# Kernel optimization log

Hardware: AMD Instinct MI355X
Metric: run time of the kernel (lower is better)

The kernel has to match this reference:

```python
import jax, jax.numpy as jnp
import numpy as np

B, HH, WW, C = 8, 56, 56, 192
DEPTH = 2
D_IN = 384      # ssm_ratio=2.0 * d_model
R = 12          # dt_rank = ceil(192/16)
HID = 768
L = HH * WW
EPS = 1e-5

PNAMES = ("norm1_w", "norm1_b", "in_proj_w", "conv_w", "conv_b", "x_proj_w",
          "dt_proj_w", "dt_proj_b", "A_log", "Ds", "out_norm_w", "out_norm_b",
          "out_proj_w", "norm2_w", "norm2_b", "fc1_w", "fc1_b", "fc2_w", "fc2_b")


def _mst_bfs_np(fm):
    """Per-image MST (Kruskal) on the 4-connected grid with cosine-distance
    edge weights mapped through exp (MinimumSpanningTree('Cosine', torch.exp)),
    then BFS from node 0. Returns (bfs order, parent-of-ordered-node)."""
    fm = np.asarray(fm, np.float32)
    Bn, H, W, Cc = fm.shape
    Ln = H * W
    idx_out = np.zeros((Bn, Ln), np.int32)
    par_out = np.zeros((Bn, Ln), np.int32)
    ids = np.arange(Ln).reshape(H, W)
    e_u = np.concatenate([ids[:, :-1].ravel(), ids[:-1, :].ravel()])
    e_v = np.concatenate([ids[:, 1:].ravel(), ids[1:, :].ravel()])
    for b in range(Bn):
        f = fm[b].reshape(Ln, Cc)
        nrm = np.linalg.norm(f, axis=1) + 1e-8
        cos = (f[e_u] * f[e_v]).sum(1) / (nrm[e_u] * nrm[e_v])
        wgt = np.exp(1.0 - cos)
        order = np.argsort(wgt, kind="stable")
        uf = np.arange(Ln)
        def find(a):
            while uf[a] != a:
                uf[a] = uf[uf[a]]
                a = uf[a]
            return a
        adj = [[] for _ in range(Ln)]
        cnt = 0
        for e in order:
            u, v = int(e_u[e]), int(e_v[e])
            ru, rv = find(u), find(v)
            if ru != rv:
                uf[ru] = rv
                adj[u].append(v)
                adj[v].append(u)
                cnt += 1
                if cnt == Ln - 1:
                    break
        bfs = np.zeros(Ln, np.int32)
        par = np.zeros(Ln, np.int32)
        visited = np.zeros(Ln, bool)
        visited[0] = True
        head, tail = 0, 1
        while head < tail:
            u = int(bfs[head])
            for v in adj[u]:
                if not visited[v]:
                    visited[v] = True
                    bfs[tail] = v
                    par[tail] = u
                    tail += 1
            head += 1
        idx_out[b] = bfs
        par_out[b] = par
    return idx_out, par_out


def _mst_bfs(x):
    shp = jax.ShapeDtypeStruct((x.shape[0], x.shape[1] * x.shape[2]), jnp.int32)
    return jax.pure_callback(_mst_bfs_np, (shp, shp), jax.lax.stop_gradient(x))


def _ln(x, w, b):
    mu = jnp.mean(x, -1, keepdims=True)
    var = jnp.mean((x - mu) ** 2, -1, keepdims=True)
    return (x - mu) * jax.lax.rsqrt(var + EPS) * w + b


def _tree_scan(feat, w, bfs_idx, bfs_par):
    # feat, w: (B, L, D); bfs_idx/bfs_par: (B, L) int32.
    # Pass 1 (leaf->root): S[p] += w[n] * S[n] in reverse BFS order.
    # Pass 2 (root->leaf): H[n] = S[n] + w[n] * (H[p] - w[n] * S[n]).
    Bn = feat.shape[0]
    bi = jnp.arange(Bn)

    def p1(S, np_):
        n, p = np_
        S = S.at[bi, p].add(w[bi, n] * S[bi, n])
        return S, None

    xs1 = (bfs_idx[:, 1:][:, ::-1].T, bfs_par[:, 1:][:, ::-1].T)
    S, _ = jax.lax.scan(p1, feat, xs1)

    def p2(Hc, np_):
        n, p = np_
        wn, sn = w[bi, n], S[bi, n]
        Hc = Hc.at[bi, n].set(sn + wn * (Hc[bi, p] - wn * sn))
        return Hc, None

    xs2 = (bfs_idx[:, 1:].T, bfs_par[:, 1:].T)
    Hh, _ = jax.lax.scan(p2, S, xs2)
    return Hh


def _layer(x, p, tree):
    bfs_idx, bfs_par = tree
    Bn = x.shape[0]
    # --- Tree_SSM branch (pre-norm) ---
    xn = _ln(x, p["norm1_w"], p["norm1_b"])
    xz = xn @ p["in_proj_w"].T                     # (B,H,W,2*D_IN)
    xs, z = jnp.split(xz, 2, axis=-1)
    xs = jax.lax.conv_general_dilated(
        xs, p["conv_w"], (1, 1), "SAME",
        dimension_numbers=("NHWC", "HWIO", "NHWC"),
        feature_group_count=D_IN) + p["conv_b"]    # depthwise 3x3
    u = jax.nn.silu(xs).reshape(Bn, L, D_IN)       # (B,L,D)
    x_dbl = u @ p["x_proj_w"].T                    # (B,L,R+2), d_state=1
    dts = jax.nn.softplus(x_dbl[..., :R] @ p["dt_proj_w"].T + p["dt_proj_b"])
    Bs, Cs = x_dbl[..., R:R + 1], x_dbl[..., R + 1:R + 2]
    A = -jnp.exp(p["A_log"][:, 0])                 # (D,)
    w = jnp.exp(dts * A)                           # edge decay to parent
    feat = dts * Bs * u                            # delta * B * u
    Hh = _tree_scan(feat, w, bfs_idx, bfs_par)
    y = (Cs * Hh + p["Ds"] * u).reshape(Bn, HH, WW, D_IN)
    y = _ln(y, p["out_norm_w"], p["out_norm_b"]) * jax.nn.silu(z)
    x = x + y @ p["out_proj_w"].T
    # --- MLP branch ---
    h = _ln(x, p["norm2_w"], p["norm2_b"])
    h = jax.nn.gelu(h @ p["fc1_w"].T + p["fc1_b"], approximate=False)
    return x + h @ p["fc2_w"].T + p["fc2_b"]


def setup_inputs() -> dict:
    key = jax.random.key(0)
    ks = jax.random.split(key, 12)
    n = jax.random.normal
    return {
        "x": n(ks[0], (B, HH, WW, C), jnp.float32),
        "norm1_w": jnp.ones((DEPTH, C)), "norm1_b": jnp.zeros((DEPTH, C)),
        "in_proj_w": n(ks[1], (DEPTH, 2 * D_IN, C)) * 0.02,
        "conv_w": n(ks[2], (DEPTH, 3, 3, 1, D_IN)) * 0.05,
        "conv_b": jnp.zeros((DEPTH, D_IN)),
        "x_proj_w": n(ks[3], (DEPTH, R + 2, D_IN)) * 0.02,
        "dt_proj_w": n(ks[4], (DEPTH, D_IN, R)) * 0.05,
        "dt_proj_b": n(ks[5], (DEPTH, D_IN)) * 0.1,
        "A_log": jnp.log(0.5 + jax.random.uniform(ks[6], (DEPTH, D_IN, 1))),
        "Ds": jax.random.uniform(ks[7], (DEPTH, D_IN)),
        "out_norm_w": jnp.ones((DEPTH, D_IN)), "out_norm_b": jnp.zeros((DEPTH, D_IN)),
        "out_proj_w": n(ks[8], (DEPTH, C, D_IN)) * 0.02,
        "norm2_w": jnp.ones((DEPTH, C)), "norm2_b": jnp.zeros((DEPTH, C)),
        "fc1_w": n(ks[9], (DEPTH, HID, C)) * 0.02, "fc1_b": jnp.zeros((DEPTH, HID)),
        "fc2_w": n(ks[10], (DEPTH, C, HID)) * 0.02, "fc2_b": jnp.zeros((DEPTH, C)),
        "fnorm_w": jnp.ones((C,)), "fnorm_b": jnp.zeros((C,)),
    }


def reference(x, norm1_w, norm1_b, in_proj_w, conv_w, conv_b, x_proj_w,
              dt_proj_w, dt_proj_b, A_log, Ds, out_norm_w, out_norm_b,
              out_proj_w, norm2_w, norm2_b, fc1_w, fc1_b, fc2_w, fc2_b,
              fnorm_w, fnorm_b):
    pvals = (norm1_w, norm1_b, in_proj_w, conv_w, conv_b, x_proj_w, dt_proj_w,
             dt_proj_b, A_log, Ds, out_norm_w, out_norm_b, out_proj_w, norm2_w,
             norm2_b, fc1_w, fc1_b, fc2_w, fc2_b)
    for i in range(DEPTH):
        pl = {k: v[i] for k, v in zip(PNAMES, pvals)}
        tree = _mst_bfs(x)  # input-adaptive MST, recomputed per layer
        x = _layer(x, pl, tree)
    return _ln(x, fnorm_w, fnorm_b)
```

## Files before the change

kernel.cpp:

```cpp
#include <hip/hip_runtime.h>
#include <math.h>

#define NB 8
#define NC 192
#define DIN 384
#define NL 3136
#define ROWS (NB*NL)
#define NE 6160
#define NHID 768

typedef unsigned short u16;
typedef unsigned int u32;
typedef unsigned long long u64;
typedef __attribute__((ext_vector_type(8))) short bh8;
typedef __attribute__((ext_vector_type(4))) float f4;

typedef __attribute__((address_space(1))) const void gl_as1;
typedef __attribute__((address_space(3))) void gl_as3;
#define GL16(g, l) __builtin_amdgcn_global_load_lds((gl_as1*)(const void*)(g), (gl_as3*)(void*)(l), 16, 0, 0)

__device__ __forceinline__ float wredsum(float v){
  v += __shfl_xor(v, 1, 64); v += __shfl_xor(v, 2, 64); v += __shfl_xor(v, 4, 64);
  v += __shfl_xor(v, 8, 64); v += __shfl_xor(v, 16, 64); v += __shfl_xor(v, 32, 64);
  return v;
}
__device__ __forceinline__ void edge_decode(int e, int& u, int& v){
  if (e < 3080){ int h = e/55, w = e - h*55; u = h*56 + w; v = u + 1; }
  else { int e2 = e - 3080; int h = e2/56, w = e2 - h*56; u = h*56 + w; v = u + 56; }
}
__device__ __forceinline__ float siluf(float x){ return x / (1.0f + expf(-x)); }
__device__ __forceinline__ float sofplus(float x){ return fmaxf(x, 0.0f) + log1pf(expf(-fabsf(x))); }
__device__ __forceinline__ float geluf(float x){ return 0.5f * x * (1.0f + erff(x * 0.70710678118654752f)); }
__device__ __forceinline__ u16 f2bf(float x){
  u32 u = __float_as_uint(x);
  u32 r = (u + 0x7fffu + ((u >> 16) & 1u)) >> 16;
  return (u16)r;
}
__device__ __forceinline__ float bf2f(u16 h){ return __uint_as_float(((u32)h) << 16); }

__global__ __launch_bounds__(256) void keysln_kernel(const float* __restrict__ x,
    const float* __restrict__ g, const float* __restrict__ bt,
    u16* __restrict__ lnout, u64* __restrict__ keys,
    const float* __restrict__ ipw, const float* __restrict__ opw,
    const float* __restrict__ f1w, const float* __restrict__ f2w,
    u16* __restrict__ ipo, u16* __restrict__ opo, u16* __restrict__ f1o, u16* __restrict__ f2o){
  int bid = blockIdx.x;
  int lane = threadIdx.x & 63;
  if (bid < 6272){
    int gw = (int)((bid * 256u + threadIdx.x) >> 6);
    const float* r = x + (size_t)gw * NC;
    float v[3]; float s = 0.f;
#pragma unroll
    for (int j = 0; j < 3; ++j){ v[j] = r[lane + 64*j]; s += v[j]; }
    s = wredsum(s);
    float mu = s * (1.0f / NC);
    float q = 0.f;
#pragma unroll
    for (int j = 0; j < 3; ++j){ float dd = v[j] - mu; q += dd*dd; }
    q = wredsum(q);
    float rs = rsqrtf(q * (1.0f / NC) + 1e-5f);
    u16* o = lnout + (size_t)gw * NC;
#pragma unroll
    for (int j = 0; j < 3; ++j){
      int dch = lane + 64*j;
      o[dch] = f2bf((v[j] - mu) * rs * g[dch] + bt[dch]);
    }
  } else if (bid < 18592){
    int gw = (int)(((bid - 6272) * 256u + threadIdx.x) >> 6);
    if (gw >= NB * NE) return;
    int b = gw / NE, e = gw - b * NE;
    int u, v; edge_decode(e, u, v);
    const float* ru = x + ((size_t)b * NL + u) * NC;
    const float* rv = x + ((size_t)b * NL + v) * NC;
    float s = 0.f, su = 0.f, sv = 0.f;
#pragma unroll
    for (int j = 0; j < 3; ++j){
      float a = ru[lane + 64*j], c = rv[lane + 64*j];
      s += a * c; su += a * a; sv += c * c;
    }
    s = wredsum(s);
    su = wredsum(su);
    sv = wredsum(sv);
    if (lane == 0){
      float nu = sqrtf(su) + 1e-8f;
      float nv = sqrtf(sv) + 1e-8f;
      float cosv = s / (nu * nv);
      float wgt = expf(1.0f - cosv);
      keys[(size_t)b*NE + e] = ((u64)__float_as_uint(wgt) << 32) | (u64)(u32)e;
    }
  } else {
    int wb = bid - 18592;
    const float* W; u16* o; int K; int nk; int base;
    if (wb < 576){ W = ipw; o = ipo; K = 192; nk = 768*192; base = wb; }
    else if (wb < 864){ W = opw; o = opo; K = 384; nk = 192*384; base = wb - 576; }
    else if (wb < 1440){ W = f1w; o = f1o; K = 192; nk = 768*192; base = wb - 864; }
    else { W = f2w; o = f2o; K = 768; nk = 192*768; base = wb - 1440; }
    int i = base*256 + threadIdx.x;
    if (i >= nk) return;
    int r = i / K, c = i - r*K;
    float v = W[i];
    u16 hi = f2bf(v);
    o[(size_t)r * 2 * K + c] = hi;
    o[(size_t)r * 2 * K + K + c] = f2bf(v - bf2f(hi));
  }
}

__device__ void tree_body(char* sm, int b, const u64* __restrict__ keys_g,
      int* __restrict__ order_g, int* __restrict__ parpos_g, int* __restrict__ pos_g,
      int* __restrict__ lvl_g, int* __restrict__ nlev_g){
  const int t = threadIdx.x;
  const int NT = 256;
  u64* best   = (u64*)sm;
  u16* parent = (u16*)(sm + 25088);
  u16* comp   = (u16*)(sm + 31360);
  u16* mstU   = (u16*)(sm + 37632);
  u16* mstV   = (u16*)(sm + 43904);
  u32* cnts   = (u32*)(sm + 56448);
  u16* adjl4  = (u16*)sm;
  u32* deg    = (u32*)(sm + 25088);

  const u64* kb = keys_g + (size_t)b * NE;
  for (int v = t; v < NL; v += NT) parent[v] = (u16)v;
  if (t == 0){ cnts[0] = 0; cnts[3] = 0xffffffffu; }
  __syncthreads();

  u32 gpass = 0;
  for (int round = 0; round < 24; ++round){
    for (int it = 0; it < 12; ++it){
      bool ch = false;
      for (int c0 = 0; c0 < NL; c0 += NT*4){
        int vv[4]; u16 pv[4]; int nb2 = 0;
#pragma unroll
        for (int j = 0; j < 4; ++j){ int v = c0 + t + j*NT; if (v < NL){ vv[nb2] = v; pv[nb2] = parent[v]; ++nb2; } }
        u16 gp[4];
        for (int j = 0; j < nb2; ++j) gp[j] = parent[pv[j]];
        for (int j = 0; j < nb2; ++j){ if (gp[j] != pv[j]){ parent[vv[j]] = gp[j]; ch = true; } }
      }
      bool docheck = (it & 1);
      if (docheck && ch) cnts[3] = gpass;
      __syncthreads();
      if (docheck){
        u32 seen = cnts[3];
        __syncthreads();
        u32 cur = gpass; ++gpass;
        if (seen != cur) break;
      }
    }
    for (int v = t; v < NL; v += NT){ comp[v] = parent[v]; best[v] = ~0ull; }
    if (t == 0) cnts[2] = 0;
    __syncthreads();
    for (int c0 = 0; c0 < NE; c0 += NT*8){
      int ee[8]; int eu[8], ev[8]; u16 cu[8], cv[8]; u64 kk[8]; int nb2 = 0;
#pragma unroll
      for (int j = 0; j < 8; ++j){
        int e = c0 + t + j*NT;
        if (e < NE){ ee[nb2] = e; int u, v; edge_decode(e, u, v); eu[nb2] = u; ev[nb2] = v; ++nb2; }
      }
      for (int j = 0; j < nb2; ++j){ cu[j] = comp[eu[j]]; cv[j] = comp[ev[j]]; }
      for (int j = 0; j < nb2; ++j){ kk[j] = kb[ee[j]]; }
      for (int j = 0; j < nb2; ++j){
        if (cu[j] != cv[j]){
          atomicMin(&best[cu[j]], kk[j]);
          atomicMin(&best[cv[j]], kk[j]);
        }
      }
    }
    __syncthreads();
    for (int c0 = 0; c0 < NL; c0 += NT*4){
      int rr[4]; u64 bk[4]; int nb2 = 0;
#pragma unroll
      for (int j = 0; j < 4; ++j){ int r = c0 + t + j*NT; if (r < NL){ rr[nb2] = r; ++nb2; } }
      u16 cr[4];
      for (int j = 0; j < nb2; ++j) cr[j] = comp[rr[j]];
      for (int j = 0; j < nb2; ++j) bk[j] = (cr[j] == (u16)rr[j]) ? best[rr[j]] : ~0ull;
      int uu[4], vv2[4]; u16 ru2[4], rv2[4];
      for (int j = 0; j < nb2; ++j){
        if (bk[j] != ~0ull){ int e = (int)(u32)bk[j]; edge_decode(e, uu[j], vv2[j]); }
      }
      for (int j = 0; j < nb2; ++j){
        if (bk[j] != ~0ull){ ru2[j] = comp[uu[j]]; rv2[j] = comp[vv2[j]]; }
      }
      for (int j = 0; j < nb2; ++j){
        if (bk[j] != ~0ull){
          int r = rr[j];
          u16 other = (ru2[j] == (u16)r) ? rv2[j] : ru2[j];
          bool mutual = (best[other] == bk[j]);
          if (!mutual || (u16)r < other){
            parent[r] = other;
            u32 id = atomicAdd(&cnts[0], 1);
            mstU[id] = (u16)uu[j]; mstV[id] = (u16)vv2[j];
            cnts[2] = 1;
          }
        }
      }
    }
    __syncthreads();
    if (cnts[0] >= (u32)(NL - 1) || cnts[2] == 0) break;
  }
  __syncthreads();

  const int nm = NL - 1;
  for (int v = t; v < NL; v += NT){
    deg[v] = 0;
    *(u64*)&adjl4[v*4] = 0xffffffffffffffffull;
  }
  __syncthreads();
  for (int c0 = 0; c0 < nm; c0 += NT*4){
    int uu[4], vv2[4]; int nb2 = 0;
#pragma unroll
    for (int j = 0; j < 4; ++j){
      int i = c0 + t + j*NT;
      if (i < nm){ uu[nb2] = mstU[i]; vv2[nb2] = mstV[i]; ++nb2; }
    }
    for (int j = 0; j < nb2; ++j){
      u32 s1 = atomicAdd(&deg[uu[j]], 1); adjl4[uu[j]*4 + s1] = (u16)vv2[j];
      u32 s2 = atomicAdd(&deg[vv2[j]], 1); adjl4[vv2[j]*4 + s2] = (u16)uu[j];
    }
  }
  __syncthreads();

  const int NARC = 2 * (NL - 1);
  u16*  arcB  = (u16*)(sm + 37632);
  u16*  nxt   = (u16*)(sm + 43908);
  u16*  rankA = (u16*)(sm + 25088);
  short* S16  = (short*)(sm + 43908);
  u16*  parA  = (u16*)(sm + 43908);
  u32*  hist  = (u32*)(sm + 25088);
  u16*  posA  = (u16*)(sm + 37632);
  u16*  dep   = (u16*)(sm + 56448);
  u32*  wsum  = (u32*)(sm + 62720);
  const int lane = t & 63, wv = t >> 6;

  {
    int dloc[13]; int st = 0;
#pragma unroll
    for (int j = 0; j < 13; ++j){
      int v = t*13 + j;
      dloc[j] = (v < NL) ? (int)deg[v] : 0;
      st += dloc[j];
    }
    int inc = st;
#pragma unroll
    for (int off = 1; off < 64; off <<= 1){
      int sh = __shfl_up(inc, off, 64);
      if (lane >= off) inc += sh;
    }
    if (lane == 63) wsum[wv] = (u32)inc;
    __syncthreads();
    int woff = 0;
    for (int k = 0; k < 4; ++k) if (k < wv) woff += (int)wsum[k];
    int run = woff + inc - st;
#pragma unroll
    for (int j = 0; j < 13; ++j){
      int v = t*13 + j;
      if (v < NL) arcB[v] = (u16)run;
      run += dloc[j];
    }
    if (t == 255) arcB[NL] = (u16)run;
  }
  __syncthreads();

  for (int idx = t; idx < NL*4; idx += NT){
    int u = idx >> 2, sl = idx & 3;
    int v = (int)adjl4[idx];
    if (v != 0xffff){
      int dv = (int)(arcB[v+1] - arcB[v]);
      int rs = 0;
#pragma unroll
      for (int j = 0; j < 4; ++j) if ((int)adjl4[v*4+j] == u) rs = j;
      int ns = rs + 1; if (ns >= dv) ns = 0;
      nxt[arcB[u] + sl] = (u16)(arcB[v] + ns);
    }
  }
  __syncthreads();
  for (int a = t; a < NARC; a += NT){
    if (nxt[a] == 0) nxt[a] = 0xffff;
  }
  __syncthreads();

  for (int a = t; a < NARC; a += NT) rankA[a] = (nxt[a] == 0xffff) ? (u16)0 : (u16)1;
  __syncthreads();
  for (int it = 0; it < 13; ++it){
    u16 nn[25], rr2[25];
#pragma unroll
    for (int k = 0; k < 25; ++k){
      int a = t + k*NT;
      nn[k] = 0xfffe; rr2[k] = 0;
      if (a < NARC){
        u16 n = nxt[a];
        if (n != 0xffff){ rr2[k] = rankA[n]; nn[k] = nxt[n]; }
      }
    }
    __syncthreads();
#pragma unroll
    for (int k = 0; k < 25; ++k){
      int a = t + k*NT;
      if (a < NARC && nn[k] != 0xfffe){
        rankA[a] = (u16)(rankA[a] + rr2[k]);
        nxt[a] = nn[k];
      }
    }
    __syncthreads();
  }

  for (int idx = t; idx < NL*4; idx += NT){
    int u = idx >> 2, sl = idx & 3;
    int v = (int)adjl4[idx];
    if (v != 0xffff){
      int a  = arcB[u] + sl;
      int rs = 0;
#pragma unroll
      for (int j = 0; j < 4; ++j) if ((int)adjl4[v*4+j] == u) rs = j;
      int ar = arcB[v] + rs;
      bool down = rankA[a] > rankA[ar];
      int pt = (NARC - 1) - (int)rankA[a];
      S16[pt] = down ? (short)1 : (short)-1;
    }
  }
  __syncthreads();

  {
    int base = t * 25;
    int vals[25]; int st = 0;
#pragma unroll
    for (int j = 0; j < 25; ++j){
      int i = base + j;
      vals[j] = (i < NARC) ? (int)S16[i] : 0;
      st += vals[j];
    }
    int inc = st;
#pragma unroll
    for (int off = 1; off < 64; off <<= 1){
      int sh = __shfl_up(inc, off, 64);
      if (lane >= off) inc += sh;
    }
    if (lane == 63) wsum[wv] = (u32)inc;
    __syncthreads();
    int woff = 0;
    for (int k = 0; k < 4; ++k) if (k < wv) woff += (int)wsum[k];
    int run = woff + inc - st;
#pragma unroll
    for (int j = 0; j < 25; ++j){
      int i = base + j;
      run += vals[j];
      if (i < NARC) S16[i] = (short)run;
    }
  }
  __syncthreads();

  if (t == 0) dep[0] = 0;
  for (int idx = t; idx < NL*4; idx += NT){
    int u = idx >> 2, sl = idx & 3;
    int v = (int)adjl4[idx];
    if (v != 0xffff){
      int a  = arcB[u] + sl;
      int rs = 0;
#pragma unroll
      for (int j = 0; j < 4; ++j) if ((int)adjl4[v*4+j] == u) rs = j;
      int ar = arcB[v] + rs;
      if (rankA[a] > rankA[ar]){
        int pt = (NARC - 1) - (int)rankA[a];
        dep[v] = (u16)S16[pt];
      }
    }
  }
  __syncthreads();

  if (t == 0) parA[0] = 0;
  for (int idx = t; idx < NL*4; idx += NT){
    int u = idx >> 2, sl = idx & 3;
    int v = (int)adjl4[idx];
    if (v != 0xffff){
      int a  = arcB[u] + sl;
      int rs = 0;
#pragma unroll
      for (int j = 0; j < 4; ++j) if ((int)adjl4[v*4+j] == u) rs = j;
      int ar = arcB[v] + rs;
      if (rankA[a] > rankA[ar]) parA[v] = (u16)u;
    }
  }
  __syncthreads();

  for (int i = t; i < NL; i += NT) hist[i] = 0;
  __syncthreads();
  int mloc = 0;
  for (int v = t; v < NL; v += NT){
    int dv = (int)dep[v];
    atomicAdd(&hist[dv], 1u);
    if (dv > mloc) mloc = dv;
  }
#pragma unroll
  for (int off = 1; off < 64; off <<= 1){
    int o = __shfl_xor(mloc, off, 64);
    if (o > mloc) mloc = o;
  }
  __syncthreads();
  if (lane == 0) wsum[wv] = (u32)mloc;
  __syncthreads();
  int maxd = 0;
  for (int k = 0; k < 4; ++k){ int x = (int)wsum[k]; if (x > maxd) maxd = x; }
  int nlev = maxd + 1;
  __syncthreads();

  {
    int hloc[13]; int st = 0;
#pragma unroll
    for (int j = 0; j < 13; ++j){
      int i2 = t*13 + j;
      hloc[j] = (i2 < NL) ? (int)hist[i2] : 0;
      st += hloc[j];
    }
    int inc = st;
#pragma unroll
    for (int off = 1; off < 64; off <<= 1){
      int sh = __shfl_up(inc, off, 64);
      if (lane >= off) inc += sh;
    }
    if (lane == 63) wsum[wv] = (u32)inc;
    __syncthreads();
    int woff = 0;
    for (int k = 0; k < 4; ++k) if (k < wv) woff += (int)wsum[k];
    int run = woff + inc - st;
#pragma unroll
    for (int j = 0; j < 13; ++j){
      int i2 = t*13 + j;
      int h = hloc[j];
      if (i2 < NL) hist[i2] = (u32)run;
      run += h;
    }
  }
  __syncthreads();
  for (int i = t; i < nlev; i += NT) lvl_g[b*3200 + i] = (int)hist[i];
  if (t == 0){ lvl_g[b*3200 + nlev] = NL; nlev_g[b] = nlev; }
  __syncthreads();

  for (int v = t; v < NL; v += NT){
    u32 p = atomicAdd(&hist[(int)dep[v]], 1u);
    posA[v] = (u16)p;
  }
  __syncthreads();

  for (int v = t; v < NL; v += NT){
    int p = (int)posA[v];
    order_g[b*NL + p] = v;
    pos_g[b*NL + v] = p;
    parpos_g[b*NL + p] = (int)posA[parA[v]];
  }
}

__device__ void inproj_body(char* sm, int bid, const u16* __restrict__ Ap, const u16* __restrict__ Wp,
                            float* __restrict__ Cm, float* __restrict__ C2){
  const int K = 192, K2 = 384;
  short* Ah = (short*)sm;
  short* Wh = (short*)(sm + 16384);
  short* Wl = (short*)(sm + 32768);
  const int bn = (bid % 6) * 128, bm = (bid / 6) * 128;
  const int tid = threadIdx.x, lane = tid & 63, wid = tid >> 6;
  const int wr = wid >> 1, wc = wid & 1;
  f4 acc[4][4];
#pragma unroll
  for (int mf = 0; mf < 4; ++mf)
#pragma unroll
    for (int nf = 0; nf < 4; ++nf) acc[mf][nf] = (f4){0.f,0.f,0.f,0.f};

  for (int k0 = 0; k0 < K; k0 += 64){
#pragma unroll
    for (int j = 0; j < 4; ++j){
      int isb = wid*4 + j;
      int r = isb*8 + (lane >> 3);
      int c = lane & 7;
      const u16* src = Ap + (size_t)(bm + r) * K + k0 + ((c ^ (r & 7)) << 3);
      GL16(src, &Ah[isb*512]);
    }
#pragma unroll
    for (int j = 0; j < 4; ++j){
      int isb = wid*4 + j;
      int r = isb*8 + (lane >> 3);
      int c = lane & 7;
      const u16* src = Wp + (size_t)(bn + r) * K2 + k0 + ((c ^ (r & 7)) << 3);
      GL16(src,     &Wh[isb*512]);
      GL16(src + K, &Wl[isb*512]);
    }
    __syncthreads();
#pragma unroll
    for (int kk = 0; kk < 2; ++kk){
      bh8 whf[4], wlf[4], ahf[4];
#pragma unroll
      for (int nf = 0; nf < 4; ++nf){
        int rw = wc*64 + nf*16 + (lane & 15);
        int c = kk*4 + (lane >> 4);
        int ad = rw*64 + ((c ^ (rw & 7)) * 8);
        whf[nf] = *(const bh8*)&Wh[ad];
        wlf[nf] = *(const bh8*)&Wl[ad];
      }
#pragma unroll
      for (int mf = 0; mf < 4; ++mf){
        int ra = wr*64 + mf*16 + (lane & 15);
        int c = kk*4 + (lane >> 4);
        int ad = ra*64 + ((c ^ (ra & 7)) * 8);
        ahf[mf] = *(const bh8*)&Ah[ad];
      }
#pragma unroll
      for (int mf = 0; mf < 4; ++mf)
#pragma unroll
        for (int nf = 0; nf < 4; ++nf){
          acc[mf][nf] = __builtin_amdgcn_mfma_f32_16x16x32_bf16(ahf[mf], whf[nf], acc[mf][nf], 0, 0, 0);
          acc[mf][nf] = __builtin_amdgcn_mfma_f32_16x16x32_bf16(ahf[mf], wlf[nf], acc[mf][nf], 0, 0, 0);
        }
    }
    __syncthreads();
  }
  const int cb = bn + wc*64;
#pragma unroll
  for (int mf = 0; mf < 4; ++mf){
    int row = bm + wr*64 + mf*16 + (lane >> 4)*4;
#pragma unroll
    for (int nf = 0; nf < 4; ++nf){
      int col = cb + nf*16 + (lane & 15);
#pragma unroll
      for (int r = 0; r < 4; ++r){
        float v = acc[mf][nf][r];
        float* op = (col < 384) ? Cm : C2;
        int oc = (col < 384) ? col : col - 384;
        op[(size_t)(row + r) * 384 + oc] = v;
      }
    }
  }
}

__global__ __launch_bounds__(256) void fused_tree_inproj(
    const u64* __restrict__ keysg, int* __restrict__ ordg, int* __restrict__ ppg,
    int* __restrict__ posg, int* __restrict__ lvlg, int* __restrict__ nlvg,
    const u16* __restrict__ Ap, const u16* __restrict__ Wp,
    float* __restrict__ Cm, float* __restrict__ C2){
  __shared__ __align__(16) char sm[62736];
  int bid = blockIdx.x;
  if (bid < 8){
    tree_body(sm, bid, keysg, ordg, ppg, posg, lvlg, nlvg);
  } else {
    inproj_body(sm, bid - 8, Ap, Wp, Cm, C2);
  }
}

__global__ __launch_bounds__(256) void sched_conv_kernel(
    const int* __restrict__ lvl_g, const int* __restrict__ nlev_g,
    u32* __restrict__ wsched_g, int* __restrict__ nwin_g,
    const float* __restrict__ xs, const float* __restrict__ cw,
    const float* __restrict__ cb, float* __restrict__ u){
  __shared__ int lvls[3200];
  int bid = blockIdx.x;
  if (bid < 8){
    int b = bid;
    int tid = threadIdx.x;
    int d = nlev_g[b];
    for (int i = tid; i <= d; i += 256) lvls[i] = lvl_g[b*3200 + i];
    __syncthreads();
    if (tid >= 64) return;
    int lane = tid;
    u32* su = wsched_g + (size_t)b*6528;
    u32* sd = su + 3264;
    int nk = d - 1;
    for (int pass = 0; pass < 2; ++pass){
      u32* out = pass ? sd : su;
      int carry = 0;
      for (int c0 = 0; c0 < nk; c0 += 64){
        int kk = c0 + lane;
        bool valid = kk < nk;
        int lo = 0, hi = 0, wc = 0;
        if (valid){
          int dd = pass ? (1 + kk) : (d - 1 - kk);
          lo = lvls[dd]; hi = lvls[dd+1];
          wc = (hi - lo + 63) >> 6;
        }
        int inc = wc;
        for (int off = 1; off < 64; off <<= 1){
          int v = __shfl_up(inc, off, 64);
          if (lane >= off) inc += v;
        }
        int excl = carry + inc - wc;
        if (valid){
          for (int w = 0; w < wc; ++w){
            int base2 = lo + (w << 6);
            u32 e = (u32)base2 | ((u32)hi << 16);
            if (base2 + 64 >= hi) e |= 0x80000000u;
            out[excl + w] = e;
          }
        }
        carry += __shfl(inc, 63, 64);
      }
      if (lane == 0) nwin_g[b*2 + pass] = carry;
    }
  } else {
    int idx = (bid - 8) * 256 + threadIdx.x;
    if (idx >= ROWS * 96) return;
    int q = idx % 96; int l = idx / 96;
    int b = l / NL; int hw = l - b * NL; int h = hw / 56; int wcc = hw - h * 56;
    int c4 = q * 4;
    float4 acc = *(const float4*)(cb + c4);
#pragma unroll
    for (int kh = 0; kh < 3; ++kh){
      int hh = h + kh - 1; if (hh < 0 || hh >= 56) continue;
#pragma unroll
      for (int kw = 0; kw < 3; ++kw){
        int wwc = wcc + kw - 1; if (wwc < 0 || wwc >= 56) continue;
        float4 iv = *(const float4*)(xs + ((size_t)(b * NL + hh*56 + wwc)) * DIN + c4);
        float4 wv = *(const float4*)(cw + (size_t)(kh*3 + kw) * DIN + c4);
        acc.x += iv.x * wv.x; acc.y += iv.y * wv.y; acc.z += iv.z * wv.z; acc.w += iv.w * wv.w;
      }
    }
    float4 o; o.x = siluf(acc.x); o.y = siluf(acc.y); o.z = siluf(acc.z); o.w = siluf(acc.w);
    *(float4*)(u + (size_t)l * DIN + c4) = o;
  }
}

template<int D, bool BF16OUT>
__global__ __launch_bounds__(256) void ln_kernel(const float* __restrict__ in, const float* __restrict__ g,
                                                 const float* __restrict__ bt, void* __restrict__ outv){
  int gw = (int)((blockIdx.x * 256u + threadIdx.x) >> 6);
  int lane = threadIdx.x & 63;
  if (gw >= ROWS) return;
  constexpr int J = D / 64;
  const float* r = in + (size_t)gw * D;
  float v[J]; float s = 0.f;
#pragma unroll
  for (int j = 0; j < J; ++j){ v[j] = r[lane + 64*j]; s += v[j]; }
  s = wredsum(s);
  float mu = s * (1.0f / D);
  float q = 0.f;
#pragma unroll
  for (int j = 0; j < J; ++j){ float dd = v[j] - mu; q += dd*dd; }
  q = wredsum(q);
  float rs = rsqrtf(q * (1.0f / D) + 1e-5f);
  if (BF16OUT){
    u16* o = (u16*)outv + (size_t)gw * D;
#pragma unroll
    for (int j = 0; j < J; ++j){
      int dch = lane + 64*j;
      float y = (v[j] - mu) * rs * g[dch] + bt[dch];
      o[dch] = f2bf(y);
    }
  } else {
    float* o = (float*)outv + (size_t)gw * D;
#pragma unroll
    for (int j = 0; j < J; ++j){ int dch = lane + 64*j; o[dch] = (v[j] - mu) * rs * g[dch] + bt[dch]; }
  }
}

template<int BN, bool BIAS, int ACT, bool RESID, bool OBF16, bool DUALOUT>
__global__ __launch_bounds__(256) void mgemm_kernel(
    const u16* __restrict__ Ap, const u16* __restrict__ Wp,
    const float* __restrict__ bias, const float* __restrict__ resid,
    float* __restrict__ Cm, float* __restrict__ C2, int M, int N, int K){
  static_assert(BN == 64 || BN == 128, "BN");
  constexpr int WT = (BN == 128) ? 64 : 32;
  constexpr int NF = WT / 16;
  __shared__ short Ah[128*64];
  __shared__ short Wh[BN*64], Wl[BN*64];
  const int bm = blockIdx.y * 128, bn = blockIdx.x * BN;
  const int tid = threadIdx.x, lane = tid & 63, wid = tid >> 6;
  const int wr = wid >> 1, wc = wid & 1;
  const int K2 = 2 * K;
  f4 acc[4][NF];
#pragma unroll
  for (int mf = 0; mf < 4; ++mf)
#pragma unroll
    for (int nf = 0; nf < NF; ++nf) acc[mf][nf] = (f4){0.f,0.f,0.f,0.f};

  for (int k0 = 0; k0 < K; k0 += 64){
#pragma unroll
    for (int j = 0; j < 4; ++j){
      int isb = wid*4 + j;
      int r = isb*8 + (lane >> 3);
      int c = lane & 7;
      const u16* src = Ap + (size_t)(bm + r) * K + k0 + ((c ^ (r & 7)) << 3);
      GL16(src, &Ah[isb*512]);
    }
#pragma unroll
    for (int j = 0; j < BN/32; ++j){
      int isb = wid*(BN/32) + j;
      int r = isb*8 + (lane >> 3);
      int c = lane & 7;
      const u16* src = Wp + (size_t)(bn + r) * K2 + k0 + ((c ^ (r & 7)) << 3);
      GL16(src,     &Wh[isb*512]);
      GL16(src + K, &Wl[isb*512]);
    }
    __syncthreads();
#pragma unroll
    for (int kk = 0; kk < 2; ++kk){
      bh8 whf[NF], wlf[NF], ahf[4];
#pragma unroll
      for (int nf = 0; nf < NF; ++nf){
        int rw = wc*WT + nf*16 + (lane & 15);
        int c = kk*4 + (lane >> 4);
        int ad = rw*64 + ((c ^ (rw & 7)) * 8);
        whf[nf] = *(const bh8*)&Wh[ad];
        wlf[nf] = *(const bh8*)&Wl[ad];
      }
#pragma unroll
      for (int mf = 0; mf < 4; ++mf){
        int ra = wr*64 + mf*16 + (lane & 15);
        int c = kk*4 + (lane >> 4);
        int ad = ra*64 + ((c ^ (ra & 7)) * 8);
        ahf[mf] = *(const bh8*)&Ah[ad];
      }
#pragma unroll
      for (int mf = 0; mf < 4; ++mf)
#pragma unroll
        for (int nf = 0; nf < NF; ++nf){
          acc[mf][nf] = __builtin_amdgcn_mfma_f32_16x16x32_bf16(ahf[mf], whf[nf], acc[mf][nf], 0, 0, 0);
          acc[mf][nf] = __builtin_amdgcn_mfma_f32_16x16x32_bf16(ahf[mf], wlf[nf], acc[mf][nf], 0, 0, 0);
        }
    }
    __syncthreads();
  }
  const int cb = bn + wc*WT;
#pragma unroll
  for (int mf = 0; mf < 4; ++mf){
    int row = bm + wr*64 + mf*16 + (lane >> 4)*4;
#pragma unroll
    for (int nf = 0; nf < NF; ++nf){
      int col = cb + nf*16 + (lane & 15);
#pragma unroll
      for (int r = 0; r < 4; ++r){
        float v = acc[mf][nf][r];
        if (BIAS) v += bias[col];
        if (ACT == 1) v = geluf(v);
        if (RESID) v += resid[(size_t)(row + r) * N + col];
        if (DUALOUT){
          float* op = (col < 384) ? Cm : C2;
          int oc = (col < 384) ? col : col - 384;
          op[(size_t)(row + r) * 384 + oc] = v;
        } else if (OBF16){
          u16* op = (u16*)Cm;
          op[(size_t)(row + r) * N + col] = f2bf(v);
        } else {
          Cm[(size_t)(row + r) * N + col] = v;
        }
      }
    }
  }
}

__global__ __launch_bounds__(256) void xdbl_kernel(const float* __restrict__ u,
    const float* __restrict__ xpw, const float* __restrict__ dtw_g,
    const float* __restrict__ dtb, const float* __restrict__ alog, const int* __restrict__ pos_g,
    float* __restrict__ wout, float* __restrict__ fout, float* __restrict__ csout){
  __shared__ float xw[14*384];
  __shared__ float dw[384*12];
  __shared__ float db[384];
  __shared__ float An[384];
  int t = threadIdx.x;
  for (int i = t; i < 14*384; i += 256) xw[i] = xpw[i];
  for (int i = t; i < 384*12; i += 256) dw[i] = dtw_g[i];
  for (int i = t; i < 384; i += 256){ db[i] = dtb[i]; An[i] = -expf(alog[i]); }
  __syncthreads();
  int wave = t >> 6, lane = t & 63;
  int row0 = blockIdx.x * 16 + wave * 4;
  for (int rr = 0; rr < 4; ++rr){
    int m = row0 + rr;
    int b = m / NL;
    int pos = pos_g[m];
    size_t orow = ((size_t)b * NL + pos) * DIN;
    const float* ur = u + (size_t)m * DIN;
    float u6[6];
#pragma unroll
    for (int j = 0; j < 6; ++j) u6[j] = ur[lane + 64*j];
    float xd[14];
#pragma unroll
    for (int r = 0; r < 14; ++r){
      float p = 0.f;
#pragma unroll
      for (int j = 0; j < 6; ++j) p += u6[j] * xw[r*384 + lane + 64*j];
      xd[r] = wredsum(p);
    }
    float Bs = xd[12], Cv = xd[13];
#pragma unroll
    for (int j = 0; j < 6; ++j){
      int dch = lane + 64*j;
      float pre = db[dch];
#pragma unroll
      for (int r = 0; r < 12; ++r) pre += xd[r] * dw[dch*12 + r];
      float dts = sofplus(pre);
      float wv = expf(dts * An[dch]);
      float fv = dts * Bs * u6[j];
      wout[orow + dch] = wv;
      fout[orow + dch] = fv;
    }
    if (lane == 0) csout[m] = Cv;
  }
}

__global__ __launch_bounds__(256) void wtr_kernel(const float* __restrict__ in, float* __restrict__ out){
  __shared__ float tile[64][65];
  int blk = blockIdx.x;
  int b = blk / (49*6);
  int r = blk - b*(49*6);
  int pt = r / 6, ct = r - pt*6;
  int t = threadIdx.x;
  int tr = t >> 6, lane = t & 63;
  const float* src = in + ((size_t)b*NL + (size_t)pt*64) * DIN + ct*64;
#pragma unroll
  for (int k = 0; k < 16; ++k){
    int rr = tr + k*4;
    tile[rr][lane] = src[(size_t)rr*DIN + lane];
  }
  __syncthreads();
  float* dst = out + ((size_t)b*DIN + (size_t)ct*64) * NL + (size_t)pt*64;
#pragma unroll
  for (int k = 0; k < 16; ++k){
    int cc = tr + k*4;
    dst[(size_t)cc*NL + lane] = tile[lane][cc];
  }
}

template<bool UP>
__device__ __forceinline__ void sweep_run(const u32* __restrict__ sc, int nw,
    float* __restrict__ Sp, const float* __restrict__ wbase, const int* __restrict__ pg, int lane){
  if (nw <= 0) return;
  u32 d0 = sc[lane];
  u32 d1 = sc[64 + lane];
  int curch = 0;
  float wA = 0.f, wB = 0.f; int pA = 0, pB = 0;
  int baseA = 0, hiA = 0, baseB = 0, hiB = 0;
  u32 eA = 0, eB = 0; bool aA = false, aB = false;
  {
    u32 dc = __shfl(d0, 0, 64);
    baseA = (int)(dc & 0xffffu); hiA = (int)((dc >> 16) & 0x7fffu); eA = dc >> 31;
    int p = baseA + lane; aA = p < hiA;
    if (aA){ wA = wbase[p]; pA = pg[p]; }
  }
  if (nw > 1){
    u32 dc = __shfl(d0, 1, 64);
    baseB = (int)(dc & 0xffffu); hiB = (int)((dc >> 16) & 0x7fffu); eB = dc >> 31;
    int p = baseB + lane; aB = p < hiB;
    if (aB){ wB = wbase[p]; pB = pg[p]; }
  }
  for (int iw = 0; iw < nw; ++iw){
    int ch = iw >> 6;
    if (ch != curch){ d0 = d1; d1 = sc[(ch + 1)*64 + lane]; curch = ch; }
    float wN = 0.f; int pN = 0; int baseN = 0, hiN = 0; u32 eN = 0; bool aN = false;
    int iw2 = iw + 2;
    if (iw2 < nw){
      int ch2 = iw2 >> 6;
      u32 dc2 = __shfl((ch2 == curch) ? d0 : d1, iw2 & 63, 64);
      baseN = (int)(dc2 & 0xffffu); hiN = (int)((dc2 >> 16) & 0x7fffu); eN = dc2 >> 31;
      int p = baseN + lane; aN = p < hiN;
      if (aN){ wN = wbase[p]; pN = pg[p]; }
    }
    int p = baseA + lane;
    if (aA){
      if (UP){
        float s = Sp[p];
        atomicAdd(&Sp[pA], wA * s);
      } else {
        float s = Sp[p]; float h = Sp[pA];
        Sp[p] = s + wA * (h - wA * s);
      }
    }
    if (eA){
      asm volatile("s_waitcnt lgkmcnt(0)" ::: "memory");
    }
    baseA = baseB; hiA = hiB; aA = aB; wA = wB; pA = pB; eA = eB;
    baseB = baseN; hiB = hiN; aB = aN; wB = wN; pB = pN; eB = eN;
  }
}

__global__ __launch_bounds__(256) void sweep8_kernel(const float* __restrict__ featp, const float* __restrict__ wtr,
    float* __restrict__ Hp, const int* __restrict__ parpos_g,
    const u32* __restrict__ wsched_g, const int* __restrict__ nwin_g){
  __shared__ float S[4*NL];
  int blk = blockIdx.x;
  int b = blk & 7, q = blk >> 3;
  int t = threadIdx.x, lane = t & 63, wv = t >> 6;
  const int* pg = parpos_g + b*NL;
  const float* fbase = featp + (size_t)b*NL*DIN + q*4;
  const float* wbase = wtr + ((size_t)b*DIN + q*4 + wv) * NL;
  float*       hbase = Hp    + (size_t)b*NL*DIN + q*4;
  for (int i = t; i < NL; i += 256){
    float4 f = *(const float4*)(fbase + (size_t)i*DIN);
    S[0*NL + i] = f.x; S[1*NL + i] = f.y; S[2*NL + i] = f.z; S[3*NL + i] = f.w;
  }
  __syncthreads();
  float* Sp = &S[wv*NL];

  const u32* su = wsched_g + (size_t)b*6528;
  const u32* sd = su + 3264;
  int nwu = nwin_g[b*2], nwd = nwin_g[b*2 + 1];
  sweep_run<true>(su, nwu, Sp, wbase, pg, lane);
  sweep_run<false>(sd, nwd, Sp, wbase, pg, lane);

  __syncthreads();
  for (int i = t; i < NL; i += 256){
    float4 o;
    o.x = S[0*NL + i]; o.y = S[1*NL + i]; o.z = S[2*NL + i]; o.w = S[3*NL + i];
    *(float4*)(hbase + (size_t)i*DIN) = o;
  }
}

__global__ __launch_bounds__(256) void ynorm_kernel(const float* __restrict__ Hp, const float* __restrict__ u,
    const float* __restrict__ z, const float* __restrict__ Cs, const int* __restrict__ order_g,
    const float* __restrict__ Ds, const float* __restrict__ g, const float* __restrict__ bt,
    u16* __restrict__ out){
  int gw = (int)((blockIdx.x * 256u + threadIdx.x) >> 6);
  int lane = threadIdx.x & 63;
  if (gw >= ROWS) return;
  int b = gw / NL;
  int node = order_g[gw];
  size_t nrow = (size_t)b * NL + node;
  float Cv = Cs[nrow];
  const float* hr = Hp + (size_t)gw * DIN;
  const float* ur = u + nrow * DIN;
  const float* zr = z + nrow * DIN;
  float y[6]; float s = 0.f;
#pragma unroll
  for (int j = 0; j < 6; ++j){
    int dch = lane + 64*j;
    y[j] = Cv * hr[dch] + Ds[dch] * ur[dch];
    s += y[j];
  }
  s = wredsum(s);
  float mu = s * (1.0f / DIN);
  float q = 0.f;
#pragma unroll
  for (int j = 0; j < 6; ++j){ float dd = y[j] - mu; q += dd*dd; }
  q = wredsum(q);
  float rs = rsqrtf(q * (1.0f / DIN) + 1e-5f);
  u16* o = out + nrow * DIN;
#pragma unroll
  for (int j = 0; j < 6; ++j){
    int dch = lane + 64*j;
    float yn = (y[j] - mu) * rs * g[dch] + bt[dch];
    float v = yn * siluf(zr[dch]);
    o[dch] = f2bf(v);
  }
}

extern "C" void kernel_launch(void* const* d_in, const int* in_sizes, int n_in,
                              void* d_out, int out_size, void* d_ws, size_t ws_size,
                              hipStream_t stream){
  const float* x_in       = (const float*)d_in[0];
  const float* norm1_w    = (const float*)d_in[1];
  const float* norm1_b    = (const float*)d_in[2];
  const float* in_proj_w  = (const float*)d_in[3];
  const float* conv_w     = (const float*)d_in[4];
  const float* conv_b     = (const float*)d_in[5];
  const float* x_proj_w   = (const float*)d_in[6];
  const float* dt_proj_w  = (const float*)d_in[7];
  const float* dt_proj_b  = (const float*)d_in[8];
  const float* A_log      = (const float*)d_in[9];
  const float* Ds         = (const float*)d_in[10];
  const float* out_norm_w = (const float*)d_in[11];
  const float* out_norm_b = (const float*)d_in[12];
  const float* out_proj_w = (const float*)d_in[13];
  const float* norm2_w    = (const float*)d_in[14];
  const float* norm2_b    = (const float*)d_in[15];
  const float* fc1_w      = (const float*)d_in[16];
  const float* fc1_b      = (const float*)d_in[17];
  const float* fc2_w      = (const float*)d_in[18];
  const float* fc2_b      = (const float*)d_in[19];
  const float* fnorm_w    = (const float*)d_in[20];
  const float* fnorm_b    = (const float*)d_in[21];

  float* ws = (float*)d_ws;
  float* X     = ws + 0;
  u16*   bufAh = (u16*)(ws + 4816896);
  float* bufZ  = ws + 9633792;
  float* bufW  = ws + 19267584;
  float* bufU  = ws + 28901376;
  float* bufF  = ws + 38535168;
  u16*   Gp    = (u16*)bufU;
  float* Csb   = ws + 48168960;
  int*   ordg  = (int*)(ws + 48194048);
  int*   ppg   = (int*)(ws + 48219136);
  int*   lvlg  = (int*)(ws + 48244224);
  int*   nlvg  = (int*)(ws + 48269824);
  u64*   keysg = (u64*)(ws + 48269832);
  u16*   ipWp  = (u16*)(ws + 48393480);
  u16*   opWp  = (u16*)(ws + 48540936);
  u16*   fc1Wp = (u16*)(ws + 48614664);
  u16*   fc2Wp = (u16*)(ws + 48762120);
  int*   posg  = (int*)(ws + 48909576);
  float* wtrp  = ws + 48934664;
  u32*   wschg = (u32*)(ws + 58568456);
  int*   nwing = (int*)(ws + 58620680);

  hipMemcpyAsync(X, x_in, (size_t)ROWS * NC * sizeof(float), hipMemcpyDeviceToDevice, stream);

  for (int i = 0; i < 2; ++i){
    keysln_kernel<<<20608, 256, 0, stream>>>(X, norm1_w + i*NC, norm1_b + i*NC, bufAh, keysg,
                                             in_proj_w + (size_t)i*NHID*NC, out_proj_w + (size_t)i*NC*DIN,
                                             fc1_w + (size_t)i*NHID*NC, fc2_w + (size_t)i*NC*NHID,
                                             ipWp, opWp, fc1Wp, fc2Wp);

    fused_tree_inproj<<<8 + 6*196, 256, 0, stream>>>(keysg, ordg, ppg, posg, lvlg, nlvg,
                                                     bufAh, ipWp, bufF, bufZ);

    sched_conv_kernel<<<8 + (ROWS*96)/256, 256, 0, stream>>>(lvlg, nlvg, wschg, nwing,
                                                             bufF, conv_w + (size_t)i*9*DIN, conv_b + i*DIN, bufU);

    xdbl_kernel<<<ROWS/16, 256, 0, stream>>>(bufU, x_proj_w + (size_t)i*14*DIN, dt_proj_w + (size_t)i*DIN*12,
                                             dt_proj_b + i*DIN, A_log + i*DIN, posg, bufW, bufF, Csb);

    wtr_kernel<<<8*49*6, 256, 0, stream>>>(bufW, wtrp);

    sweep8_kernel<<<NB*96, 256, 0, stream>>>(bufF, wtrp, bufF, ppg, wschg, nwing);

    ynorm_kernel<<<ROWS/4, 256, 0, stream>>>(bufF, bufU, bufZ, Csb, ordg, Ds + i*DIN,
                                             out_norm_w + i*DIN, out_norm_b + i*DIN, (u16*)bufW);

    mgemm_kernel<64,false,0,true,false,false><<<dim3(3,196), 256, 0, stream>>>((u16*)bufW, opWp, nullptr, X, X, nullptr, ROWS, 192, 384);

    ln_kernel<192,true><<<ROWS/4, 256, 0, stream>>>(X, norm2_w + i*NC, norm2_b + i*NC, bufAh);
    mgemm_kernel<128,true,1,false,true,false><<<dim3(6,196), 256, 0, stream>>>(bufAh, fc1Wp, fc1_b + i*NHID, nullptr, (float*)Gp, nullptr, ROWS, NHID, 192);
    mgemm_kernel<64,true,0,true,false,false><<<dim3(3,196), 256, 0, stream>>>(Gp, fc2Wp, fc2_b + i*NC, X, X, nullptr, ROWS, 192, 768);
  }

  ln_kernel<192,false><<<ROWS/4, 256, 0, stream>>>(X, fnorm_w, fnorm_b, d_out);
}
```

Measured before the change: 1.293 ms.

## Replace serial downward tree sweep with pointer-jumping parallel scan

The downward (root-to-leaf) pass of the tree scan, previously a level-by-level serial sweep inside the sweep kernel, becomes a separate kernel. It uses pointer doubling over the parent array, with 12 rounds of ancestor tables precomputed in the schedule kernel. Each node's affine recurrence (a + b*parent) is composed in log depth, trading many dependent levels for about 12 fully parallel LDS rounds per channel pair. This adds an extra kernel launch, extra global traffic for Hp and the ancestor tables, and more total arithmetic.

```diff
diff --git a/kernel.cpp b/kernel.cpp
--- a/kernel.cpp
+++ b/kernel.cpp
@@ -544,10 +544,12 @@
 
 __global__ __launch_bounds__(256) void sched_conv_kernel(
     const int* __restrict__ lvl_g, const int* __restrict__ nlev_g,
-    u32* __restrict__ wsched_g, int* __restrict__ nwin_g,
+    const int* __restrict__ parpos_g,
+    u32* __restrict__ wsched_g, int* __restrict__ nwin_g, u16* __restrict__ par2k_g,
     const float* __restrict__ xs, const float* __restrict__ cw,
     const float* __restrict__ cb, float* __restrict__ u){
   __shared__ int lvls[3200];
+  __shared__ u16 pj[2][NL];
   int bid = blockIdx.x;
   if (bid < 8){
     int b = bid;
@@ -555,40 +557,57 @@
     int d = nlev_g[b];
     for (int i = tid; i <= d; i += 256) lvls[i] = lvl_g[b*3200 + i];
     __syncthreads();
-    if (tid >= 64) return;
-    int lane = tid;
-    u32* su = wsched_g + (size_t)b*6528;
-    u32* sd = su + 3264;
-    int nk = d - 1;
-    for (int pass = 0; pass < 2; ++pass){
-      u32* out = pass ? sd : su;
-      int carry = 0;
-      for (int c0 = 0; c0 < nk; c0 += 64){
-        int kk = c0 + lane;
-        bool valid = kk < nk;
-        int lo = 0, hi = 0, wc = 0;
-        if (valid){
-          int dd = pass ? (1 + kk) : (d - 1 - kk);
-          lo = lvls[dd]; hi = lvls[dd+1];
-          wc = (hi - lo + 63) >> 6;
+    if (tid < 64){
+      int lane = tid;
+      u32* su = wsched_g + (size_t)b*6528;
+      u32* sd = su + 3264;
+      int nk = d - 1;
+      for (int pass = 0; pass < 2; ++pass){
+        u32* out = pass ? sd : su;
+        int carry = 0;
+        for (int c0 = 0; c0 < nk; c0 += 64){
+          int kk = c0 + lane;
+          bool valid = kk < nk;
+          int lo = 0, hi = 0, wc = 0;
+          if (valid){
+            int dd = pass ? (1 + kk) : (d - 1 - kk);
+            lo = lvls[dd]; hi = lvls[dd+1];
+            wc = (hi - lo + 63) >> 6;
+          }
+          int inc = wc;
+          for (int off = 1; off < 64; off <<= 1){
+            int v = __shfl_up(inc, off, 64);
+            if (lane >= off) inc += v;
+          }
+          int excl = carry + inc - wc;
+          if (valid){
+            for (int w = 0; w < wc; ++w){
+              int base2 = lo + (w << 6);
+              u32 e = (u32)base2 | ((u32)hi << 16);
+              if (base2 + 64 >= hi) e |= 0x80000000u;
+              out[excl + w] = e;
+            }
+          }
+          carry += __shfl(inc, 63, 64);
         }
-        int inc = wc;
-        for (int off = 1; off < 64; off <<= 1){
-          int v = __shfl_up(inc, off, 64);
-          if (lane >= off) inc += v;
-        }
-        int excl = carry + inc - wc;
-        if (valid){
-          for (int w = 0; w < wc; ++w){
-            int base2 = lo + (w << 6);
-            u32 e = (u32)base2 | ((u32)hi << 16);
-            if (base2 + 64 >= hi) e |= 0x80000000u;
-            out[excl + w] = e;
-          }
-        }
-        carry += __shfl(inc, 63, 64);
-      }
-      if (lane == 0) nwin_g[b*2 + pass] = carry;
+        if (lane == 0) nwin_g[b*2 + pass] = carry;
+      }
+    }
+    const int* ppb = parpos_g + b*NL;
+    for (int p = tid; p < NL; p += 256) pj[0][p] = (u16)ppb[p];
+    __syncthreads();
+    {
+      u16* tb0 = par2k_g + ((size_t)b*12 + 0)*NL;
+      for (int p = tid; p < NL; p += 256) tb0[p] = pj[0][p];
+    }
+    int cur = 0;
+    for (int r = 1; r < 12; ++r){
+      for (int p = tid; p < NL; p += 256) pj[cur^1][p] = pj[cur][pj[cur][p]];
+      __syncthreads();
+      cur ^= 1;
+      u16* tbr = par2k_g + ((size_t)b*12 + r)*NL;
+      for (int p = tid; p < NL; p += 256) tbr[p] = pj[cur][p];
+      __syncthreads();
     }
   } else {
     int idx = (bid - 8) * 256 + threadIdx.x;
@@ -813,8 +832,7 @@
   }
 }
 
-template<bool UP>
-__device__ __forceinline__ void sweep_run(const u32* __restrict__ sc, int nw,
+__device__ __forceinline__ void sweep_run_up(const u32* __restrict__ sc, int nw,
     float* __restrict__ Sp, const float* __restrict__ wbase, const int* __restrict__ pg, int lane){
   if (nw <= 0) return;
   u32 d0 = sc[lane];
@@ -849,13 +867,8 @@
     }
     int p = baseA + lane;
     if (aA){
-      if (UP){
-        float s = Sp[p];
-        atomicAdd(&Sp[pA], wA * s);
-      } else {
-        float s = Sp[p]; float h = Sp[pA];
-        Sp[p] = s + wA * (h - wA * s);
-      }
+      float s = Sp[p];
+      atomicAdd(&Sp[pA], wA * s);
     }
     if (eA){
       asm volatile("s_waitcnt lgkmcnt(0)" ::: "memory");
@@ -865,7 +878,7 @@
   }
 }
 
-__global__ __launch_bounds__(256) void sweep8_kernel(const float* __restrict__ featp, const float* __restrict__ wtr,
+__global__ __launch_bounds__(256) void sweepup_kernel(const float* __restrict__ featp, const float* __restrict__ wtr,
     float* __restrict__ Hp, const int* __restrict__ parpos_g,
     const u32* __restrict__ wsched_g, const int* __restrict__ nwin_g){
   __shared__ float S[4*NL];
@@ -884,16 +897,67 @@
   float* Sp = &S[wv*NL];
 
   const u32* su = wsched_g + (size_t)b*6528;
-  const u32* sd = su + 3264;
-  int nwu = nwin_g[b*2], nwd = nwin_g[b*2 + 1];
-  sweep_run<true>(su, nwu, Sp, wbase, pg, lane);
-  sweep_run<false>(sd, nwd, Sp, wbase, pg, lane);
+  int nwu = nwin_g[b*2];
+  sweep_run_up(su, nwu, Sp, wbase, pg, lane);
 
   __syncthreads();
   for (int i = t; i < NL; i += 256){
     float4 o;
     o.x = S[0*NL + i]; o.y = S[1*NL + i]; o.z = S[2*NL + i]; o.w = S[3*NL + i];
     *(float4*)(hbase + (size_t)i*DIN) = o;
+  }
+}
+
+__global__ __launch_bounds__(256) void downp_kernel(float* __restrict__ Hp, const float* __restrict__ wtr,
+    const u16* __restrict__ par2k_g){
+  __shared__ float aA[2*NL];
+  __shared__ float bB[2*NL];
+  int blk = blockIdx.x;
+  int b = blk & 7, cp = blk >> 3;
+  int ch0 = cp*2;
+  int t = threadIdx.x;
+  const float* w0p = wtr + ((size_t)b*DIN + ch0)*NL;
+  const float* w1p = w0p + NL;
+  float* hb = Hp + (size_t)b*NL*DIN + ch0;
+  for (int p = t; p < NL; p += 256){
+    float2 s = *(const float2*)(hb + (size_t)p*DIN);
+    float w0 = w0p[p], w1 = w1p[p];
+    bool root = (p == 0);
+    aA[p]      = root ? s.x : s.x*(1.f - w0*w0);
+    bB[p]      = root ? 0.f : w0;
+    aA[NL + p] = root ? s.y : s.y*(1.f - w1*w1);
+    bB[NL + p] = root ? 0.f : w1;
+  }
+  __syncthreads();
+  const u16* tb = par2k_g + (size_t)b*12*NL;
+  for (int r = 0; r < 12; ++r){
+    const u16* tr2 = tb + (size_t)r*NL;
+    float na0[13], nb0[13], na1[13], nb1[13];
+#pragma unroll
+    for (int k = 0; k < 13; ++k){
+      int p = t + k*256;
+      if (p < NL){
+        int pp = (int)tr2[p];
+        float a0 = aA[p],     b0 = bB[p],     pa0 = aA[pp],     pb0 = bB[pp];
+        float a1 = aA[NL+p],  b1 = bB[NL+p],  pa1 = aA[NL+pp],  pb1 = bB[NL+pp];
+        na0[k] = a0 + b0*pa0; nb0[k] = b0*pb0;
+        na1[k] = a1 + b1*pa1; nb1[k] = b1*pb1;
+      }
+    }
+    __syncthreads();
+#pragma unroll
+    for (int k = 0; k < 13; ++k){
+      int p = t + k*256;
+      if (p < NL){
+        aA[p] = na0[k];    bB[p] = nb0[k];
+        aA[NL+p] = na1[k]; bB[NL+p] = nb1[k];
+      }
+    }
+    __syncthreads();
+  }
+  for (int p = t; p < NL; p += 256){
+    float2 o; o.x = aA[p]; o.y = aA[NL + p];
+    *(float2*)(hb + (size_t)p*DIN) = o;
   }
 }
 
@@ -983,6 +1047,7 @@
   float* wtrp  = ws + 48934664;
   u32*   wschg = (u32*)(ws + 58568456);
   int*   nwing = (int*)(ws + 58620680);
+  u16*   par2k = (u16*)(ws + 58620696);
 
   hipMemcpyAsync(X, x_in, (size_t)ROWS * NC * sizeof(float), hipMemcpyDeviceToDevice, stream);
 
@@ -995,7 +1060,7 @@
     fused_tree_inproj<<<8 + 6*196, 256, 0, stream>>>(keysg, ordg, ppg, posg, lvlg, nlvg,
                                                      bufAh, ipWp, bufF, bufZ);
 
-    sched_conv_kernel<<<8 + (ROWS*96)/256, 256, 0, stream>>>(lvlg, nlvg, wschg, nwing,
+    sched_conv_kernel<<<8 + (ROWS*96)/256, 256, 0, stream>>>(lvlg, nlvg, ppg, wschg, nwing, par2k,
                                                              bufF, conv_w + (size_t)i*9*DIN, conv_b + i*DIN, bufU);
 
     xdbl_kernel<<<ROWS/16, 256, 0, stream>>>(bufU, x_proj_w + (size_t)i*14*DIN, dt_proj_w + (size_t)i*DIN*12,
@@ -1003,7 +1068,9 @@
 
     wtr_kernel<<<8*49*6, 256, 0, stream>>>(bufW, wtrp);
 
-    sweep8_kernel<<<NB*96, 256, 0, stream>>>(bufF, wtrp, bufF, ppg, wschg, nwing);
+    sweepup_kernel<<<NB*96, 256, 0, stream>>>(bufF, wtrp, bufF, ppg, wschg, nwing);
+
+    downp_kernel<<<8*192, 256, 0, stream>>>(bufF, wtrp, par2k);
 
     ynorm_kernel<<<ROWS/4, 256, 0, stream>>>(bufF, bufU, bufZ, Csb, ordg, Ds + i*DIN,
                                              out_norm_w + i*DIN, out_norm_b + i*DIN, (u16*)bufW);
```

After: 1.335 ms. 1.03x slower.
